# Kernel tuning notes

Hardware: AMD Instinct MI355X
Metric: run time of the kernel (lower is better)

The kernel has to match this reference:

```python
import jax, jax.numpy as jnp
import numpy as np

N = 30000       # mesh nodes
E = 150000      # mesh edges
L = 128         # latent_size
STEPS = 5       # message_passing_steps
TW = 5          # time_window
TD = 2          # target_dim
NODE_IN = TD + 1 + 9   # u + load + node_type one-hot = 12
EDGE_IN = 2 + 1 + TD   # rel_mesh + dist + grad_u = 5


def _mlp(x, W1, b1, W2, b2, g, be):
    # Linear -> ReLU -> Linear -> ReLU -> LayerNorm (matches MLP module)
    h = jax.nn.relu(x @ W1 + b1)
    h = jax.nn.relu(h @ W2 + b2)
    mu = jnp.mean(h, axis=-1, keepdims=True)
    var = jnp.mean(jnp.square(h - mu), axis=-1, keepdims=True)
    return g * (h - mu) / jnp.sqrt(var + 1e-5) + be


def setup_inputs() -> dict:
    key = jax.random.key(0)
    ks = iter(jax.random.split(key, 64))
    def nrm(shape, s=0.05):
        return jax.random.normal(next(ks), shape, dtype=jnp.float32) * s
    inp = {}
    inp['mesh_pos'] = jax.random.normal(next(ks), (1, N, 2), dtype=jnp.float32)
    inp['node_type'] = jax.random.normal(next(ks), (1, N, 9), dtype=jnp.float32)
    inp['u'] = jax.random.normal(next(ks), (1, N, TD), dtype=jnp.float32)
    inp['load'] = jax.random.normal(next(ks), (1, N, 1), dtype=jnp.float32)
    inp['senders'] = jax.random.randint(next(ks), (E,), 0, N, dtype=jnp.int32)
    inp['receivers'] = jax.random.randint(next(ks), (E,), 0, N, dtype=jnp.int32)
    # node encoder MLP(12 -> 128)
    inp['enc_node_W1'] = nrm((NODE_IN, L)); inp['enc_node_b1'] = nrm((L,), 0.01)
    inp['enc_node_W2'] = nrm((L, L));       inp['enc_node_b2'] = nrm((L,), 0.01)
    inp['enc_node_g'] = jnp.ones((L,), jnp.float32); inp['enc_node_be'] = jnp.zeros((L,), jnp.float32)
    # edge encoder MLP(5 -> 128)
    inp['enc_edge_W1'] = nrm((EDGE_IN, L)); inp['enc_edge_b1'] = nrm((L,), 0.01)
    inp['enc_edge_W2'] = nrm((L, L));       inp['enc_edge_b2'] = nrm((L,), 0.01)
    inp['enc_edge_g'] = jnp.ones((L,), jnp.float32); inp['enc_edge_be'] = jnp.zeros((L,), jnp.float32)
    # STEPS GraphNetBlocks, params stacked along leading axis for lax.scan
    inp['blk_edge_W1'] = nrm((STEPS, 3 * L, L)); inp['blk_edge_b1'] = nrm((STEPS, L), 0.01)
    inp['blk_edge_W2'] = nrm((STEPS, L, L));     inp['blk_edge_b2'] = nrm((STEPS, L), 0.01)
    inp['blk_edge_g'] = jnp.ones((STEPS, L), jnp.float32); inp['blk_edge_be'] = jnp.zeros((STEPS, L), jnp.float32)
    inp['blk_node_W1'] = nrm((STEPS, 2 * L, L)); inp['blk_node_b1'] = nrm((STEPS, L), 0.01)
    inp['blk_node_W2'] = nrm((STEPS, L, L));     inp['blk_node_b2'] = nrm((STEPS, L), 0.01)
    inp['blk_node_g'] = jnp.ones((STEPS, L), jnp.float32); inp['blk_node_be'] = jnp.zeros((STEPS, L), jnp.float32)
    # decoder: Conv1d(L,8,1) -> Swish -> Conv1d(8, TD*TW, 1); kernel-size-1 conv == per-node linear
    inp['dec_W1'] = nrm((L, 8)); inp['dec_b1'] = nrm((8,), 0.01)
    inp['dec_W2'] = nrm((8, TD * TW)); inp['dec_b2'] = nrm((TD * TW,), 0.01)
    return inp


def reference(mesh_pos, node_type, u, load, senders, receivers,
              enc_node_W1, enc_node_b1, enc_node_W2, enc_node_b2, enc_node_g, enc_node_be,
              enc_edge_W1, enc_edge_b1, enc_edge_W2, enc_edge_b2, enc_edge_g, enc_edge_be,
              blk_edge_W1, blk_edge_b1, blk_edge_W2, blk_edge_b2, blk_edge_g, blk_edge_be,
              blk_node_W1, blk_node_b1, blk_node_W2, blk_node_b2, blk_node_g, blk_node_be,
              dec_W1, dec_b1, dec_W2, dec_b2):
    # --- encode ---
    node_feats = jnp.concatenate([u, load, node_type], axis=-1)        # [1,N,12]
    nl = _mlp(node_feats, enc_node_W1, enc_node_b1, enc_node_W2, enc_node_b2, enc_node_g, enc_node_be)
    rel = mesh_pos[:, senders] - mesh_pos[:, receivers]                # [1,E,2]
    dist = jnp.linalg.norm(rel, axis=-1, keepdims=True)                # [1,E,1]
    grad_u = u[:, senders] - u[:, receivers]                           # [1,E,2]
    ef = jnp.concatenate([rel, dist, grad_u], axis=-1)                 # [1,E,5]
    el = _mlp(ef, enc_edge_W1, enc_edge_b1, enc_edge_W2, enc_edge_b2, enc_edge_g, enc_edge_be)
    n_nodes = nl.shape[1]

    # --- process: GraphNetBlocks with residual connections ---
    def block(carry, p):
        nl, el = carry
        edge_in = jnp.concatenate([nl[:, senders], nl[:, receivers], el], axis=-1)  # [1,E,3L]
        ne = _mlp(edge_in, p['eW1'], p['eb1'], p['eW2'], p['eb2'], p['eg'], p['ebe'])
        aggr = jax.vmap(lambda e: jax.ops.segment_sum(e, receivers, num_segments=n_nodes))(ne)  # [1,N,L]
        node_in = jnp.concatenate([nl, aggr], axis=-1)                 # [1,N,2L]
        nn = _mlp(node_in, p['nW1'], p['nb1'], p['nW2'], p['nb2'], p['ng'], p['nbe'])
        return (nl + nn, el + ne), None

    ps = {'eW1': blk_edge_W1, 'eb1': blk_edge_b1, 'eW2': blk_edge_W2, 'eb2': blk_edge_b2,
          'eg': blk_edge_g, 'ebe': blk_edge_be,
          'nW1': blk_node_W1, 'nb1': blk_node_b1, 'nW2': blk_node_W2, 'nb2': blk_node_b2,
          'ng': blk_node_g, 'nbe': blk_node_be}
    (nl, el), _ = jax.lax.scan(block, (nl, el), ps)

    # --- decode (1x1 Conv1d == per-node linear) ---
    h = nl @ dec_W1 + dec_b1
    h = h * jax.nn.sigmoid(h)                                          # Swish(beta=1)
    decoded = h @ dec_W2 + dec_b2                                      # [1,N,TW*TD]
    dt = jnp.repeat(jnp.arange(1, TW + 1, dtype=decoded.dtype), TD)    # [TW*TD]
    delta = (decoded * dt).reshape(-1, TW, TD).transpose(1, 0, 2)      # [TW,N,TD]
    return delta
```

## Files before the change

kernel.cpp:

```cpp
#include <hip/hip_runtime.h>
#include <hip/hip_bf16.h>

#define LNUM 128
#define NNODES 30000
#define NEDGES 150000
#define NSTEPS 5


typedef _Float16 f16;
typedef __attribute__((ext_vector_type(8))) _Float16 f16x8;
typedef __attribute__((ext_vector_type(4))) float f32x4;

__device__ __forceinline__ void glds16(const void* g, void* l) {
    __builtin_amdgcn_global_load_lds(
        (const __attribute__((address_space(1))) void*)g,
        (__attribute__((address_space(3))) void*)l, 16, 0, 0);
}

template<int ROWS, int K, int KP>
__device__ __forceinline__ void mlp_apply(
    const float* __restrict__ xs, float* __restrict__ hv,
    float* __restrict__ mu_s, float* __restrict__ rs_s,
    const float* __restrict__ W1, const float* __restrict__ b1,
    const float* __restrict__ W2, const float* __restrict__ b2,
    const float* __restrict__ g,  const float* __restrict__ be,
    float out[ROWS])
{
    const int t = threadIdx.x;
    float acc[ROWS];
    {
        const float bb = b1[t];
        #pragma unroll
        for (int r = 0; r < ROWS; r++) acc[r] = bb;
    }
    int k = 0;
    for (; k + 4 <= K; k += 4) {
        const float w0 = W1[(k + 0) * LNUM + t];
        const float w1 = W1[(k + 1) * LNUM + t];
        const float w2 = W1[(k + 2) * LNUM + t];
        const float w3 = W1[(k + 3) * LNUM + t];
        #pragma unroll
        for (int r = 0; r < ROWS; r++) {
            const float4 x = *(const float4*)(xs + r * KP + k);
            acc[r] = fmaf(x.x, w0, acc[r]);
            acc[r] = fmaf(x.y, w1, acc[r]);
            acc[r] = fmaf(x.z, w2, acc[r]);
            acc[r] = fmaf(x.w, w3, acc[r]);
        }
    }
    for (; k < K; ++k) {
        const float w = W1[k * LNUM + t];
        #pragma unroll
        for (int r = 0; r < ROWS; r++) acc[r] = fmaf(xs[r * KP + k], w, acc[r]);
    }
    #pragma unroll
    for (int r = 0; r < ROWS; r++) hv[r * LNUM + t] = fmaxf(acc[r], 0.f);
    __syncthreads();
    {
        const float bb = b2[t];
        #pragma unroll
        for (int r = 0; r < ROWS; r++) acc[r] = bb;
    }
    for (int k2 = 0; k2 < LNUM; k2 += 4) {
        const float w0 = W2[(k2 + 0) * LNUM + t];
        const float w1 = W2[(k2 + 1) * LNUM + t];
        const float w2 = W2[(k2 + 2) * LNUM + t];
        const float w3 = W2[(k2 + 3) * LNUM + t];
        #pragma unroll
        for (int r = 0; r < ROWS; r++) {
            const float4 x = *(const float4*)(hv + r * LNUM + k2);
            acc[r] = fmaf(x.x, w0, acc[r]);
            acc[r] = fmaf(x.y, w1, acc[r]);
            acc[r] = fmaf(x.z, w2, acc[r]);
            acc[r] = fmaf(x.w, w3, acc[r]);
        }
    }
    __syncthreads();
    #pragma unroll
    for (int r = 0; r < ROWS; r++) hv[r * LNUM + t] = fmaxf(acc[r], 0.f);
    __syncthreads();
    if (t < ROWS) {
        float s = 0.f, s2 = 0.f;
        for (int kk = 0; kk < LNUM; kk++) {
            const float v = hv[t * LNUM + kk];
            s += v; s2 += v * v;
        }
        const float m = s * (1.0f / LNUM);
        mu_s[t] = m;
        rs_s[t] = rsqrtf(fmaxf(s2 * (1.0f / LNUM) - m * m, 0.f) + 1e-5f);
    }
    __syncthreads();
    const float gg = g[t], bbe = be[t];
    #pragma unroll
    for (int r = 0; r < ROWS; r++)
        out[r] = fmaf(gg * (hv[r * LNUM + t] - mu_s[r]), rs_s[r], bbe);
}

__global__ __launch_bounds__(128) void encode_nodes_k(
    const float* __restrict__ u, const float* __restrict__ load_,
    const float* __restrict__ ntype,
    const float* __restrict__ W1, const float* __restrict__ b1,
    const float* __restrict__ W2, const float* __restrict__ b2,
    const float* __restrict__ g,  const float* __restrict__ be,
    f16* __restrict__ nl)
{
    constexpr int ROWS = 4, K = 12, KP = 12;
    __shared__ __align__(16) float xs[ROWS * KP];
    __shared__ __align__(16) float hv[ROWS * LNUM];
    __shared__ float mu_s[ROWS], rs_s[ROWS];
    const int t = threadIdx.x;
    const int base = blockIdx.x * ROWS;
    if (t < ROWS * K) {
        const int r = t / K, k = t % K;
        const int n = base + r;
        float v;
        if (k < 2)      v = u[n * 2 + k];
        else if (k < 3) v = load_[n];
        else            v = ntype[n * 9 + (k - 3)];
        xs[r * KP + k] = v;
    }
    __syncthreads();
    float out[ROWS];
    mlp_apply<ROWS, K, KP>(xs, hv, mu_s, rs_s, W1, b1, W2, b2, g, be, out);
    #pragma unroll
    for (int r = 0; r < ROWS; r++) nl[(base + r) * LNUM + t] = (f16)out[r];
}

#define PE1 245760
#define PE2 81920
#define PN1 163840
#define PN2 81920
#define PQ1 4096
#define PQ2 16384
#define PTOT (PE1+PE2+PN1+PN2+PQ1+PQ2)

__global__ __launch_bounds__(256) void prep_w_all_k(
    const float* __restrict__ eW1, const float* __restrict__ eW2,
    const float* __restrict__ nW1, const float* __restrict__ nW2,
    const float* __restrict__ qW1, const float* __restrict__ qW2,
    f16* __restrict__ out)
{
    int j = blockIdx.x * 256 + threadIdx.x;
    if (j >= PTOT) return;
    const float* W; int K, kreal; f16* hi; f16* p = out;
    if (j < PE1) { W = eW1; K = 384; kreal = 384; hi = p; }
    else { p += PE1; j -= PE1;
    if (j < PE2) { W = eW2; K = 128; kreal = 128; hi = p; }
    else { p += PE2; j -= PE2;
    if (j < PN1) { W = nW1; K = 256; kreal = 256; hi = p; }
    else { p += PN1; j -= PN1;
    if (j < PN2) { W = nW2; K = 128; kreal = 128; hi = p; }
    else { p += PN2; j -= PN2;
    if (j < PQ1) { W = qW1; K = 32;  kreal = 5;   hi = p; }
    else { p += PQ1; j -= PQ1;
         { W = qW2; K = 128; kreal = 128; hi = p; } } } } } }
    const int k = j % K;
    const int rem = j / K;
    const int n = rem & 127;
    const int s = rem >> 7;
    const float v = (k < kreal) ? W[((size_t)s * kreal + k) * 128 + n] : 0.f;
    hi[j] = (f16)v;
}

template<int MODE, int NCH1, int K1S>
__global__ __launch_bounds__(256, 6) void mfma_mlp_k(
    const f16* __restrict__ Lat, const float* __restrict__ Fa,
    const float* __restrict__ Fb,
    f16* __restrict__ io, float* __restrict__ aggr,
    const int* __restrict__ senders, const int* __restrict__ receivers,
    const f16* __restrict__ W1h, const float* __restrict__ b1,
    const f16* __restrict__ W2h, const float* __restrict__ b2,
    const float* __restrict__ gam, const float* __restrict__ bet,
    int nrows)
{
    __shared__ __align__(16) f16 WH[4096];
    __shared__ __align__(16) unsigned short Yh[64 * 128];

    const int t  = threadIdx.x;
    const int w  = t >> 6;
    const int l  = t & 63;
    const int lr = l & 15;
    const int lg = l >> 4;
    const int swz = lg ^ ((lr >> 1) & 3);
    const int base = blockIdx.x * 64;

    const int eg  = base + w * 16 + lr;
    const int egc = min(eg, nrows - 1);

    int sv = 0, rv = 0;
    if constexpr (MODE != 1) { sv = senders[egc]; rv = receivers[egc]; }

    float feat[8];
    if constexpr (MODE == 2) {
        const float ax = Fa[sv * 2], ay = Fa[sv * 2 + 1];
        const float bx = Fa[rv * 2], by = Fa[rv * 2 + 1];
        const float rx = ax - bx, ry = ay - by;
        feat[0] = rx; feat[1] = ry; feat[2] = sqrtf(rx * rx + ry * ry);
        feat[3] = Fb[sv * 2] - Fb[rv * 2];
        feat[4] = Fb[sv * 2 + 1] - Fb[rv * 2 + 1];
        feat[5] = 0.f; feat[6] = 0.f; feat[7] = 0.f;
    }

    auto stage = [&](const f16* __restrict__ Wh, const int kst, const int kc) {
        #pragma unroll
        for (int i = 0; i < 2; i++) {
            const int c = 2 * w + i;
            const int ophys = c * 1024 + l * 16;
            const int olog  = ophys ^ (((ophys >> 7) & 3) << 4);
            const int row   = olog >> 6;
            const int slot  = (olog >> 4) & 3;
            glds16(Wh + (size_t)row * kst + kc * 32 + slot * 8, (char*)WH + c * 1024);
        }
    };

    uint4 qn;
    float xn[8];
    auto prefetch = [&](int kc) {
        if constexpr (MODE == 0) {
            const f16* src;
            if (kc < 4)      src = Lat + (size_t)sv  * 128 + kc * 32 + lg * 8;
            else if (kc < 8) src = Lat + (size_t)rv  * 128 + (kc - 4) * 32 + lg * 8;
            else             src = io  + (size_t)egc * 128 + (kc - 8) * 32 + lg * 8;
            qn = *(const uint4*)src;
        } else if constexpr (MODE == 1) {
            if (kc < 4) {
                qn = *(const uint4*)(io + (size_t)egc * 128 + kc * 32 + lg * 8);
            } else {
                const float* s = Fa + (size_t)egc * 128 + (kc - 4) * 32 + lg * 8;
                const float4 a = *(const float4*)s;
                const float4 b = *(const float4*)(s + 4);
                xn[0] = a.x; xn[1] = a.y; xn[2] = a.z; xn[3] = a.w;
                xn[4] = b.x; xn[5] = b.y; xn[6] = b.z; xn[7] = b.w;
            }
        }
    };

    const f32x4 zero4 = {0.f, 0.f, 0.f, 0.f};
    f32x4 acc[8];
    #pragma unroll
    for (int mf = 0; mf < 8; mf++) acc[mf] = zero4;

    prefetch(0);

    #pragma unroll
    for (int kc = 0; kc < NCH1; ++kc) {
        __syncthreads();
        stage(W1h, K1S, kc);
        const bool isF16 = (MODE == 0) || (MODE == 1 && kc < 4);
        f16x8 XHv, XLv;
        bool useXL = false;
        if constexpr (MODE == 2) {
            union { f16 h[8]; f16x8 v; } uh, ul;
            #pragma unroll
            for (int j = 0; j < 8; j++) {
                const float x = (lg == 0) ? feat[j] : 0.f;
                const f16 h = (f16)x;
                uh.h[j] = h;
                ul.h[j] = (f16)(x - (float)h);
            }
            XHv = uh.v; XLv = ul.v; useXL = true;
        } else if (isF16) {
            union { uint4 q; f16x8 v; } cc; cc.q = qn;
            XHv = cc.v;
        } else {
            union { f16 h[8]; f16x8 v; } uh, ul;
            #pragma unroll
            for (int j = 0; j < 8; j++) {
                const f16 h = (f16)xn[j];
                uh.h[j] = h;
                ul.h[j] = (f16)(xn[j] - (float)h);
            }
            XHv = uh.v; XLv = ul.v; useXL = true;
        }
        __syncthreads();
        if (kc + 1 < NCH1) prefetch(kc + 1);
        #pragma unroll
        for (int mf = 0; mf < 8; mf++) {
            const int off = (mf * 16 + lr) * 64 + (swz << 4);
            const f16x8 wh = *(const f16x8*)((const char*)WH + off);
            acc[mf] = __builtin_amdgcn_mfma_f32_16x16x32_f16(XHv, wh, acc[mf], 0, 0, 0);
            if (useXL)
                acc[mf] = __builtin_amdgcn_mfma_f32_16x16x32_f16(XLv, wh, acc[mf], 0, 0, 0);
        }
    }

    #pragma unroll
    for (int mf = 0; mf < 8; mf++) {
        const float bb1 = b1[mf * 16 + lr];
        #pragma unroll
        for (int reg = 0; reg < 4; reg++) {
            float v = acc[mf][reg] + bb1;
            v = fmaxf(v, 0.f);
            union { f16 h; unsigned short u; } cc; cc.h = (f16)v;
            const int row = w * 16 + lg * 4 + reg;
            const int cb  = (mf * 16 + lr) * 2;
            *(unsigned short*)((char*)Yh + row * 256 +
                               (cb ^ (((lg * 4 + reg) & 7) << 4))) = cc.u;
        }
        acc[mf] = zero4;
    }

    #pragma unroll
    for (int kc = 0; kc < 4; ++kc) {
        __syncthreads();
        stage(W2h, 128, kc);
        union { uint4 q; f16x8 v; } YH;
        {
            const int row = w * 16 + lr;
            const int cb  = (kc * 32 + lg * 8) * 2;
            YH.q = *(const uint4*)((const char*)Yh + row * 256 +
                                   (cb ^ ((lr & 7) << 4)));
        }
        __syncthreads();
        #pragma unroll
        for (int mf = 0; mf < 8; mf++) {
            const int off = (mf * 16 + lr) * 64 + (swz << 4);
            const f16x8 wh = *(const f16x8*)((const char*)WH + off);
            acc[mf] = __builtin_amdgcn_mfma_f32_16x16x32_f16(YH.v, wh, acc[mf], 0, 0, 0);
        }
    }

    float vv[8][4];
    float s1[4] = {0, 0, 0, 0}, s2[4] = {0, 0, 0, 0};
    #pragma unroll
    for (int mf = 0; mf < 8; mf++) {
        const float bb2 = b2[mf * 16 + lr];
        #pragma unroll
        for (int reg = 0; reg < 4; reg++) {
            float v = acc[mf][reg] + bb2;
            v = fmaxf(v, 0.f);
            vv[mf][reg] = v;
            s1[reg] += v; s2[reg] += v * v;
        }
    }
    #pragma unroll
    for (int m = 1; m < 16; m <<= 1) {
        #pragma unroll
        for (int reg = 0; reg < 4; reg++) {
            s1[reg] += __shfl_xor(s1[reg], m);
            s2[reg] += __shfl_xor(s2[reg], m);
        }
    }
    float gg[8], b8[8];
    #pragma unroll
    for (int mf = 0; mf < 8; mf++) {
        gg[mf] = gam[mf * 16 + lr];
        b8[mf] = bet[mf * 16 + lr];
    }

    #pragma unroll
    for (int reg = 0; reg < 4; reg++) {
        const float mu = s1[reg] * (1.f / 128.f);
        const float rs = rsqrtf(fmaxf(s2[reg] * (1.f / 128.f) - mu * mu, 0.f) + 1e-5f);
        const int row = w * 16 + lg * 4 + reg;
        const int idx = base + row;
        if (idx < nrows) {
            if constexpr (MODE == 0) {
                const int rc = receivers[idx];
                #pragma unroll
                for (int mf = 0; mf < 8; mf++) {
                    const int col = mf * 16 + lr;
                    const float o = gg[mf] * (vv[mf][reg] - mu) * rs + b8[mf];
                    atomicAdd(&aggr[(size_t)rc * 128 + col], o);
                    f16* p = io + (size_t)idx * 128 + col;
                    *p = (f16)((float)*p + o);
                }
            } else if constexpr (MODE == 1) {
                #pragma unroll
                for (int mf = 0; mf < 8; mf++) {
                    const int col = mf * 16 + lr;
                    const float o = gg[mf] * (vv[mf][reg] - mu) * rs + b8[mf];
                    f16* p = io + (size_t)idx * 128 + col;
                    *p = (f16)((float)*p + o);
                }
            } else {
                #pragma unroll
                for (int mf = 0; mf < 8; mf++) {
                    const int col = mf * 16 + lr;
                    const float o = gg[mf] * (vv[mf][reg] - mu) * rs + b8[mf];
                    io[(size_t)idx * 128 + col] = (f16)o;
                }
            }
        }
    }
}

__global__ __launch_bounds__(128) void decode_k(
    const f16* __restrict__ nl,
    const float* __restrict__ W1, const float* __restrict__ b1,
    const float* __restrict__ W2, const float* __restrict__ b2,
    float* __restrict__ out)
{
    constexpr int NPB = 16;
    __shared__ __align__(16) float xs[NPB * LNUM];
    __shared__ float hh[NPB * 8];
    const int t = threadIdx.x;
    const int base = blockIdx.x * NPB;
    for (int r = 0; r < NPB; r++) xs[r * LNUM + t] = (float)nl[(base + r) * LNUM + t];
    __syncthreads();
    {
        const int node = t >> 3, j = t & 7;
        float a = b1[j];
        for (int k = 0; k < LNUM; k++) a = fmaf(xs[node * LNUM + k], W1[k * 8 + j], a);
        hh[node * 8 + j] = a / (1.f + expf(-a));
    }
    __syncthreads();
    for (int idx = t; idx < NPB * 10; idx += 128) {
        const int node = idx / 10, c = idx % 10;
        float a = b2[c];
        #pragma unroll
        for (int j = 0; j < 8; j++) a = fmaf(hh[node * 8 + j], W2[j * 10 + c], a);
        const int tt = c >> 1, d = c & 1;
        out[(size_t)tt * (NNODES * 2) + (size_t)(base + node) * 2 + d] =
            a * (float)(tt + 1);
    }
}

__global__ __launch_bounds__(256) void zero_k(float* __restrict__ p, int n)
{
    const int i = blockIdx.x * 256 + threadIdx.x;
    if (i < n) p[i] = 0.f;
}

extern "C" void kernel_launch(void* const* d_in, const int* in_sizes, int n_in,
                              void* d_out, int out_size, void* d_ws, size_t ws_size,
                              hipStream_t stream) {
    const float* F[34];
    for (int i = 0; i < 34; i++) F[i] = (const float*)d_in[i];
    const int* senders   = (const int*)d_in[4];
    const int* receivers = (const int*)d_in[5];

    const size_t nN = (size_t)NNODES * LNUM;
    const size_t nE = (size_t)NEDGES * LNUM;
    f16* nl16 = (f16*)d_ws;
    f16* el16 = nl16 + nN;
    float* aggr = (float*)(el16 + nE);
    f16* wb = (f16*)(aggr + nN);
    f16 *eW1h = wb;
    f16 *eW2h = eW1h + PE1;
    f16 *nW1h = eW2h + PE2;
    f16 *nW2h = nW1h + PN1;
    f16 *qW1h = nW2h + PN2;
    f16 *qW2h = qW1h + PQ1;

    prep_w_all_k<<<(PTOT + 255) / 256, 256, 0, stream>>>(
        F[18], F[20], F[24], F[26], F[12], F[14], wb);

    encode_nodes_k<<<NNODES / 4, 128, 0, stream>>>(
        F[2], F[3], F[1], F[6], F[7], F[8], F[9], F[10], F[11], nl16);

    const int egrid = (NEDGES + 63) / 64;
    const int ngrid = (NNODES + 63) / 64;

    mfma_mlp_k<2, 1, 32><<<egrid, 256, 0, stream>>>(
        nullptr, F[0], F[2], el16, nullptr, senders, receivers,
        qW1h, F[13], qW2h, F[15], F[16], F[17], NEDGES);

    for (int s = 0; s < NSTEPS; s++) {
        zero_k<<<(NNODES * LNUM + 255) / 256, 256, 0, stream>>>(aggr, NNODES * LNUM);
        mfma_mlp_k<0, 12, 384><<<egrid, 256, 0, stream>>>(
            nl16, nullptr, nullptr, el16, aggr, senders, receivers,
            eW1h + (size_t)s * 384 * 128, F[19] + s * LNUM,
            eW2h + (size_t)s * 128 * 128, F[21] + s * LNUM,
            F[22] + s * LNUM, F[23] + s * LNUM, NEDGES);
        mfma_mlp_k<1, 8, 256><<<ngrid, 256, 0, stream>>>(
            nullptr, aggr, nullptr, nl16, nullptr, nullptr, nullptr,
            nW1h + (size_t)s * 256 * 128, F[25] + s * LNUM,
            nW2h + (size_t)s * 128 * 128, F[27] + s * LNUM,
            F[28] + s * LNUM, F[29] + s * LNUM, NNODES);
    }

    decode_k<<<NNODES / 16, 128, 0, stream>>>(
        nl16, F[30], F[31], F[32], F[33], (float*)d_out);
}
```

Before: 793.7 us.

## Store edge aggregation buffer in fp16 with packed two-wide atomic adds

The per-node aggregation buffer changes from fp32 to fp16. Edge-kernel scatter now pairs adjacent columns through a lane shuffle and issues one packed v2f16 atomic add per pair, which halves both the atomic count and the bytes moved. The node kernel reads the aggregate as fp16 directly, so the hi/lo split and its second MFMA pass go away, and the zeroing kernel clears half as much memory. The cost is accuracy: fp16 accumulation of scattered sums loses precision and can overflow or drift compared with fp32 atomics.

Result: no change. 787.1 us (-0.8%).

```diff
diff --git a/kernel.cpp b/kernel.cpp
--- a/kernel.cpp
+++ b/kernel.cpp
@@ -8,6 +8,7 @@
 
 
 typedef _Float16 f16;
+typedef __attribute__((ext_vector_type(2))) _Float16 f16x2;
 typedef __attribute__((ext_vector_type(8))) _Float16 f16x8;
 typedef __attribute__((ext_vector_type(4))) float f32x4;
 
@@ -15,6 +16,23 @@
     __builtin_amdgcn_global_load_lds(
         (const __attribute__((address_space(1))) void*)g,
         (__attribute__((address_space(3))) void*)l, 16, 0, 0);
+}
+
+__device__ __forceinline__ void atomic_pk_add(f16* addr, f16 lo, f16 hi) {
+#if __has_builtin(__builtin_amdgcn_global_atomic_fadd_v2f16)
+    f16x2 v; v[0] = lo; v[1] = hi;
+    __builtin_amdgcn_global_atomic_fadd_v2f16(
+        (__attribute__((address_space(1))) f16x2*)addr, v);
+#else
+    uint32_t* p = (uint32_t*)addr;
+    uint32_t old = *p, assumed;
+    do {
+        assumed = old;
+        union { uint32_t u; f16 h[2]; } c; c.u = assumed;
+        c.h[0] += lo; c.h[1] += hi;
+        old = atomicCAS(p, assumed, c.u);
+    } while (old != assumed);
+#endif
 }
 
 template<int ROWS, int K, int KP>
@@ -166,7 +184,7 @@
 __global__ __launch_bounds__(256, 6) void mfma_mlp_k(
     const f16* __restrict__ Lat, const float* __restrict__ Fa,
     const float* __restrict__ Fb,
-    f16* __restrict__ io, float* __restrict__ aggr,
+    f16* __restrict__ io, f16* __restrict__ aggr,
     const int* __restrict__ senders, const int* __restrict__ receivers,
     const f16* __restrict__ W1h, const float* __restrict__ b1,
     const f16* __restrict__ W2h, const float* __restrict__ b2,
@@ -214,7 +232,6 @@
     };
 
     uint4 qn;
-    float xn[8];
     auto prefetch = [&](int kc) {
         if constexpr (MODE == 0) {
             const f16* src;
@@ -223,15 +240,10 @@
             else             src = io  + (size_t)egc * 128 + (kc - 8) * 32 + lg * 8;
             qn = *(const uint4*)src;
         } else if constexpr (MODE == 1) {
-            if (kc < 4) {
-                qn = *(const uint4*)(io + (size_t)egc * 128 + kc * 32 + lg * 8);
-            } else {
-                const float* s = Fa + (size_t)egc * 128 + (kc - 4) * 32 + lg * 8;
-                const float4 a = *(const float4*)s;
-                const float4 b = *(const float4*)(s + 4);
-                xn[0] = a.x; xn[1] = a.y; xn[2] = a.z; xn[3] = a.w;
-                xn[4] = b.x; xn[5] = b.y; xn[6] = b.z; xn[7] = b.w;
-            }
+            const f16* src;
+            if (kc < 4) src = io  + (size_t)egc * 128 + kc * 32 + lg * 8;
+            else        src = Lat + (size_t)egc * 128 + (kc - 4) * 32 + lg * 8;
+            qn = *(const uint4*)src;
         }
     };
 
@@ -246,7 +258,6 @@
     for (int kc = 0; kc < NCH1; ++kc) {
         __syncthreads();
         stage(W1h, K1S, kc);
-        const bool isF16 = (MODE == 0) || (MODE == 1 && kc < 4);
         f16x8 XHv, XLv;
         bool useXL = false;
         if constexpr (MODE == 2) {
@@ -259,18 +270,9 @@
                 ul.h[j] = (f16)(x - (float)h);
             }
             XHv = uh.v; XLv = ul.v; useXL = true;
-        } else if (isF16) {
+        } else {
             union { uint4 q; f16x8 v; } cc; cc.q = qn;
             XHv = cc.v;
-        } else {
-            union { f16 h[8]; f16x8 v; } uh, ul;
-            #pragma unroll
-            for (int j = 0; j < 8; j++) {
-                const f16 h = (f16)xn[j];
-                uh.h[j] = h;
-                ul.h[j] = (f16)(xn[j] - (float)h);
-            }
-            XHv = uh.v; XLv = ul.v; useXL = true;
         }
         __syncthreads();
         if (kc + 1 < NCH1) prefetch(kc + 1);
@@ -361,7 +363,10 @@
                 for (int mf = 0; mf < 8; mf++) {
                     const int col = mf * 16 + lr;
                     const float o = gg[mf] * (vv[mf][reg] - mu) * rs + b8[mf];
-                    atomicAdd(&aggr[(size_t)rc * 128 + col], o);
+                    const float op = __shfl_xor(o, 1);
+                    if ((lr & 1) == 0)
+                        atomic_pk_add(aggr + (size_t)rc * 128 + col,
+                                      (f16)o, (f16)op);
                     f16* p = io + (size_t)idx * 128 + col;
                     *p = (f16)((float)*p + o);
                 }
@@ -432,10 +437,10 @@
 
     const size_t nN = (size_t)NNODES * LNUM;
     const size_t nE = (size_t)NEDGES * LNUM;
-    f16* nl16 = (f16*)d_ws;
-    f16* el16 = nl16 + nN;
-    float* aggr = (float*)(el16 + nE);
-    f16* wb = (f16*)(aggr + nN);
+    f16* nl16   = (f16*)d_ws;
+    f16* el16   = nl16 + nN;
+    f16* aggr16 = el16 + nE;
+    f16* wb     = aggr16 + nN;
     f16 *eW1h = wb;
     f16 *eW2h = eW1h + PE1;
     f16 *nW1h = eW2h + PE2;
@@ -457,14 +462,15 @@
         qW1h, F[13], qW2h, F[15], F[16], F[17], NEDGES);
 
     for (int s = 0; s < NSTEPS; s++) {
-        zero_k<<<(NNODES * LNUM + 255) / 256, 256, 0, stream>>>(aggr, NNODES * LNUM);
+        zero_k<<<(NNODES * 64 + 255) / 256, 256, 0, stream>>>(
+            (float*)aggr16, NNODES * 64);
         mfma_mlp_k<0, 12, 384><<<egrid, 256, 0, stream>>>(
-            nl16, nullptr, nullptr, el16, aggr, senders, receivers,
+            nl16, nullptr, nullptr, el16, aggr16, senders, receivers,
             eW1h + (size_t)s * 384 * 128, F[19] + s * LNUM,
             eW2h + (size_t)s * 128 * 128, F[21] + s * LNUM,
             F[22] + s * LNUM, F[23] + s * LNUM, NEDGES);
         mfma_mlp_k<1, 8, 256><<<ngrid, 256, 0, stream>>>(
-            nullptr, aggr, nullptr, nl16, nullptr, nullptr, nullptr,
+            aggr16, nullptr, nullptr, nl16, nullptr, nullptr, nullptr,
             nW1h + (size_t)s * 256 * 128, F[25] + s * LNUM,
             nW2h + (size_t)s * 128 * 128, F[27] + s * LNUM,
             F[28] + s * LNUM, F[29] + s * LNUM, NNODES);
```
